# Optimization experiments

Hardware: AMD Instinct MI355X
Metric: run time of the kernel (lower is better)

## Reference

```python
import jax, jax.numpy as jnp
import numpy as np

B, T_ENC, T_DEC = 8, 1024, 100
DMODEL, H, DK, DV, DFF = 512, 8, 64, 64, 2048
L_ENC, L_DEC = 2, 2
EPS = 1e-5
MASK_FILL = -1e10  # original code masked_fills the post-softmax probs with -1e10


def _ln(x, g, b):
    m = jnp.mean(x, -1, keepdims=True)
    v = jnp.mean(jnp.square(x - m), -1, keepdims=True)
    return (x - m) * jax.lax.rsqrt(v + EPS) * g + b


def _mha(Q, K, V, Wq, Wk, Wv, causal):
    Bz, Lq, _ = Q.shape
    Lk = K.shape[1]
    q = (Q @ Wq).reshape(Bz, Lq, H, DK).transpose(0, 2, 1, 3)  # b h q d
    k = (K @ Wk).reshape(Bz, Lk, H, DK).transpose(0, 2, 1, 3)
    v = (V @ Wv).reshape(Bz, Lk, H, DV).transpose(0, 2, 1, 3)
    scores = jnp.einsum('bhqd,bhkd->bhqk', q, k) * (1.0 / np.float32(np.sqrt(DK)))
    p = jax.nn.softmax(scores, axis=-1)
    if causal:
        # faithful to original: mask applied AFTER softmax, fill value -1e10
        mask = jnp.tril(jnp.ones((Lq, Lk), dtype=bool))
        p = jnp.where(mask[None, None], p, jnp.float32(MASK_FILL))
    o = jnp.einsum('bhqk,bhkd->bhqd', p, v)
    return o.transpose(0, 2, 1, 3).reshape(Bz, Lq, H * DV)


def setup_inputs() -> dict:
    key = jax.random.key(0)
    ks = iter(jax.random.split(key, 64))
    s = 0.02
    d = {
        'x': jax.random.normal(next(ks), (B, T_ENC, DMODEL), jnp.float32),
        'y': jax.random.normal(next(ks), (B, T_DEC, DMODEL), jnp.float32),
    }
    def w(shape):
        return jax.random.normal(next(ks), shape, jnp.float32) * s
    # encoder params, stacked over layers
    d['enc_Wq'] = w((L_ENC, DMODEL, DMODEL)); d['enc_Wk'] = w((L_ENC, DMODEL, H * DK))
    d['enc_Wv'] = w((L_ENC, DMODEL, H * DV))
    d['enc_ff_w1'] = w((L_ENC, DMODEL, DFF)); d['enc_ff_b1'] = jnp.zeros((L_ENC, DFF))
    d['enc_ff_w2'] = w((L_ENC, DFF, DMODEL)); d['enc_ff_b2'] = jnp.zeros((L_ENC, DMODEL))
    d['enc_ln1_g'] = jnp.ones((L_ENC, DMODEL)); d['enc_ln1_b'] = jnp.zeros((L_ENC, DMODEL))
    d['enc_ln2_g'] = jnp.ones((L_ENC, DMODEL)); d['enc_ln2_b'] = jnp.zeros((L_ENC, DMODEL))
    # decoder params
    d['dec_Wq1'] = w((L_DEC, DMODEL, DMODEL)); d['dec_Wk1'] = w((L_DEC, DMODEL, H * DK))
    d['dec_Wv1'] = w((L_DEC, DMODEL, H * DV))
    d['dec_Wq2'] = w((L_DEC, DMODEL, DMODEL)); d['dec_Wk2'] = w((L_DEC, DMODEL, H * DK))
    d['dec_Wv2'] = w((L_DEC, DMODEL, H * DV))
    d['dec_ff_w1'] = w((L_DEC, DMODEL, DFF)); d['dec_ff_b1'] = jnp.zeros((L_DEC, DFF))
    d['dec_ff_w2'] = w((L_DEC, DFF, DMODEL)); d['dec_ff_b2'] = jnp.zeros((L_DEC, DMODEL))
    d['dec_ln1_g'] = jnp.ones((L_DEC, DMODEL)); d['dec_ln1_b'] = jnp.zeros((L_DEC, DMODEL))
    d['dec_ln2_g'] = jnp.ones((L_DEC, DMODEL)); d['dec_ln2_b'] = jnp.zeros((L_DEC, DMODEL))
    d['dec_ln3_g'] = jnp.ones((L_DEC, DMODEL)); d['dec_ln3_b'] = jnp.zeros((L_DEC, DMODEL))
    return d


def reference(x, y,
              enc_Wq, enc_Wk, enc_Wv, enc_ff_w1, enc_ff_b1, enc_ff_w2, enc_ff_b2,
              enc_ln1_g, enc_ln1_b, enc_ln2_g, enc_ln2_b,
              dec_Wq1, dec_Wk1, dec_Wv1, dec_Wq2, dec_Wk2, dec_Wv2,
              dec_ff_w1, dec_ff_b1, dec_ff_w2, dec_ff_b2,
              dec_ln1_g, dec_ln1_b, dec_ln2_g, dec_ln2_b, dec_ln3_g, dec_ln3_b):
    # encoder stacks
    for i in range(L_ENC):
        att = _mha(x, x, x, enc_Wq[i], enc_Wk[i], enc_Wv[i], causal=False)
        x1 = _ln(x + att, enc_ln1_g[i], enc_ln1_b[i])
        ff = jax.nn.relu(x1 @ enc_ff_w1[i] + enc_ff_b1[i]) @ enc_ff_w2[i] + enc_ff_b2[i]
        x = _ln(x1 + ff, enc_ln2_g[i], enc_ln2_b[i])
    # decoder stacks
    for i in range(L_DEC):
        a1 = _mha(y, y, y, dec_Wq1[i], dec_Wk1[i], dec_Wv1[i], causal=True)
        y1 = _ln(y + a1, dec_ln1_g[i], dec_ln1_b[i])
        a2 = _mha(y1, x, x, dec_Wq2[i], dec_Wk2[i], dec_Wv2[i], causal=False)
        y2 = _ln(y1 + a2, dec_ln2_g[i], dec_ln2_b[i])
        ff = jax.nn.relu(y2 @ dec_ff_w1[i] + dec_ff_b1[i]) @ dec_ff_w2[i] + dec_ff_b2[i]
        y = _ln(y2 + ff, dec_ln3_g[i], dec_ln3_b[i])
    return y
```

## Files before the change

### kernel.cpp

```cpp
#include <hip/hip_runtime.h>
#include <cstddef>

typedef unsigned short u16;
typedef __attribute__((ext_vector_type(8))) short bf16x8;
typedef __attribute__((ext_vector_type(4))) float f32x4;

__device__ __forceinline__ u16 f2b(float f) {
    union { float f; unsigned u; } x; x.f = f;
    unsigned r = x.u + 0x7FFFu + ((x.u >> 16) & 1u);
    return (u16)(r >> 16);
}
__device__ __forceinline__ float b2f(u16 v) {
    union { unsigned u; float f; } x; x.u = ((unsigned)v) << 16;
    return x.f;
}

__device__ __forceinline__ void gload_lds16(const u16* g, u16* l) {
    __builtin_amdgcn_global_load_lds(
        (const __attribute__((address_space(1))) void*)g,
        (__attribute__((address_space(3))) void*)l, 16, 0, 0);
}

__global__ __launch_bounds__(256) void gemm_mfma_kernel(
    const u16* __restrict__ A, const u16* __restrict__ Bt,
    const float* __restrict__ bias,
    float* __restrict__ Cf, u16* __restrict__ Cb,
    int M, int K, int N, int relu)
{
    __shared__ __align__(16) u16 As[128 * 32];
    __shared__ __align__(16) u16 Bs[128 * 32];

    const int tid  = threadIdx.x;
    const int wave = tid >> 6;
    const int lane = tid & 63;
    const int m0 = blockIdx.y * 128;
    const int n0 = blockIdx.x * 128;

    const int wm = (wave & 1) * 64;
    const int wn = (wave >> 1) * 64;

    const int srow  = lane >> 2;
    const int skoff = (lane & 3) * 8;

    f32x4 acc[4][4];
#pragma unroll
    for (int i = 0; i < 4; ++i)
#pragma unroll
        for (int j = 0; j < 4; ++j)
            acc[i][j] = (f32x4){0.f, 0.f, 0.f, 0.f};

    const int fm = lane & 15;
    const int fk = (lane >> 4) * 8;

    for (int k0 = 0; k0 < K; k0 += 32) {
        __syncthreads();
        {
            const int r0 = wave * 32;
            int gr0 = m0 + r0 + srow;       if (gr0 >= M) gr0 = M - 1;
            int gr1 = m0 + r0 + 16 + srow;  if (gr1 >= M) gr1 = M - 1;
            gload_lds16(A + (size_t)gr0 * K + k0 + skoff, &As[(r0) * 32]);
            gload_lds16(A + (size_t)gr1 * K + k0 + skoff, &As[(r0 + 16) * 32]);
            gload_lds16(Bt + (size_t)(n0 + r0 + srow) * K + k0 + skoff, &Bs[(r0) * 32]);
            gload_lds16(Bt + (size_t)(n0 + r0 + 16 + srow) * K + k0 + skoff, &Bs[(r0 + 16) * 32]);
        }
        __syncthreads();

        bf16x8 af[4], bfr[4];
#pragma unroll
        for (int t = 0; t < 4; ++t) {
            af[t]  = *(const bf16x8*)(&As[(wm + t * 16 + fm) * 32 + fk]);
            bfr[t] = *(const bf16x8*)(&Bs[(wn + t * 16 + fm) * 32 + fk]);
        }
#pragma unroll
        for (int i = 0; i < 4; ++i)
#pragma unroll
            for (int j = 0; j < 4; ++j)
                acc[i][j] = __builtin_amdgcn_mfma_f32_16x16x32_bf16(
                    af[i], bfr[j], acc[i][j], 0, 0, 0);
    }

    const int col = lane & 15;
    const int rq  = (lane >> 4) * 4;
#pragma unroll
    for (int j = 0; j < 4; ++j) {
        const int gn = n0 + wn + j * 16 + col;
        const float bb = bias ? bias[gn] : 0.f;
#pragma unroll
        for (int i = 0; i < 4; ++i) {
            const int gmb = m0 + wm + i * 16 + rq;
#pragma unroll
            for (int r = 0; r < 4; ++r) {
                const int gm = gmb + r;
                if (gm < M) {
                    float v = acc[i][j][r] + bb;
                    if (relu) v = fmaxf(v, 0.f);
                    if (Cb) Cb[(size_t)gm * N + gn] = f2b(v);
                    else    Cf[(size_t)gm * N + gn] = v;
                }
            }
        }
    }
}

__global__ __launch_bounds__(256) void gemm64_kernel(
    const u16* __restrict__ A, const u16* __restrict__ Bt,
    const float* __restrict__ bias,
    float* __restrict__ Cf, u16* __restrict__ Cb,
    int M, int K, int N, int relu)
{
    __shared__ __align__(16) u16 As[64 * 32];
    __shared__ __align__(16) u16 Bs[64 * 32];

    const int tid  = threadIdx.x;
    const int wave = tid >> 6;
    const int lane = tid & 63;
    const int m0 = blockIdx.y * 64;
    const int n0 = blockIdx.x * 64;
    const int wm = (wave & 1) * 32;
    const int wn = (wave >> 1) * 32;

    const int srow  = lane >> 2;
    const int skoff = (lane & 3) * 8;

    f32x4 acc[2][2];
#pragma unroll
    for (int i = 0; i < 2; ++i)
#pragma unroll
        for (int j = 0; j < 2; ++j) acc[i][j] = (f32x4){0.f, 0.f, 0.f, 0.f};

    const int fm = lane & 15;
    const int fk = (lane >> 4) * 8;

    for (int k0 = 0; k0 < K; k0 += 32) {
        __syncthreads();
        {
            int gr = m0 + wave * 16 + srow; if (gr >= M) gr = M - 1;
            gload_lds16(A + (size_t)gr * K + k0 + skoff, &As[(wave * 16) * 32]);
            gload_lds16(Bt + (size_t)(n0 + wave * 16 + srow) * K + k0 + skoff,
                        &Bs[(wave * 16) * 32]);
        }
        __syncthreads();

        bf16x8 af[2], bfr[2];
#pragma unroll
        for (int t = 0; t < 2; ++t) {
            af[t]  = *(const bf16x8*)(&As[(wm + t * 16 + fm) * 32 + fk]);
            bfr[t] = *(const bf16x8*)(&Bs[(wn + t * 16 + fm) * 32 + fk]);
        }
#pragma unroll
        for (int i = 0; i < 2; ++i)
#pragma unroll
            for (int j = 0; j < 2; ++j)
                acc[i][j] = __builtin_amdgcn_mfma_f32_16x16x32_bf16(
                    af[i], bfr[j], acc[i][j], 0, 0, 0);
    }

    const int col = lane & 15;
    const int rq  = (lane >> 4) * 4;
#pragma unroll
    for (int j = 0; j < 2; ++j) {
        const int gn = n0 + wn + j * 16 + col;
        const float bb = bias ? bias[gn] : 0.f;
#pragma unroll
        for (int i = 0; i < 2; ++i) {
            const int gmb = m0 + wm + i * 16 + rq;
#pragma unroll
            for (int r = 0; r < 4; ++r) {
                const int gm = gmb + r;
                if (gm < M) {
                    float v = acc[i][j][r] + bb;
                    if (relu) v = fmaxf(v, 0.f);
                    if (Cb) Cb[(size_t)gm * N + gn] = f2b(v);
                    else    Cf[(size_t)gm * N + gn] = v;
                }
            }
        }
    }
}

__global__ __launch_bounds__(256) void attn_mfma_kernel(
    const u16* __restrict__ Qp, const u16* __restrict__ Kp,
    const u16* __restrict__ Vp, u16* __restrict__ Op,
    int Lq, int Lk, int ldq, int ldkv, int ldo)
{
    const int q0 = blockIdx.x * 128;
    const int h  = blockIdx.y;
    const int b  = blockIdx.z;
    const int tid  = threadIdx.x;
    const int wave = tid >> 6;
    const int lane = tid & 63;
    const int c = lane & 15;
    const int g = lane >> 4;
    const float scale = 0.125f;

    __shared__ __align__(16) u16 Ks[64 * 72];
    __shared__ __align__(16) u16 Vs[64 * 72];
    __shared__ __align__(16) u16 Ps[128 * 72];

    bf16x8 aq[2][2];
#pragma unroll
    for (int half = 0; half < 2; ++half) {
        int qrow = q0 + wave * 32 + half * 16 + c;
        if (qrow > Lq - 1) qrow = Lq - 1;
        const u16* src = Qp + ((size_t)(b * Lq + qrow)) * ldq + h * 64 + g * 8;
        aq[half][0] = *(const bf16x8*)(src);
        aq[half][1] = *(const bf16x8*)(src + 32);
    }

    float den[2][4] = {};
    f32x4 o[2][4];
#pragma unroll
    for (int half = 0; half < 2; ++half)
#pragma unroll
        for (int j = 0; j < 4; ++j) o[half][j] = (f32x4){0.f, 0.f, 0.f, 0.f};

    const int srow = tid & 63;
    const int sseg = tid >> 6;

    for (int t = 0; t < (Lk >> 6); ++t) {
        const int k0 = t << 6;
        __syncthreads();
        {
            const u16* kg = Kp + ((size_t)(b * Lk + k0 + srow)) * ldkv + h * 64;
            *(bf16x8*)(&Ks[srow * 72 + sseg * 8])      = *(const bf16x8*)(kg + sseg * 8);
            *(bf16x8*)(&Ks[srow * 72 + 32 + sseg * 8]) = *(const bf16x8*)(kg + 32 + sseg * 8);
            const u16* vg = Vp + ((size_t)(b * Lk + k0 + srow)) * ldkv + h * 64;
            bf16x8 v0 = *(const bf16x8*)(vg + sseg * 8);
            bf16x8 v1 = *(const bf16x8*)(vg + 32 + sseg * 8);
#pragma unroll
            for (int i = 0; i < 8; ++i) {
                Vs[(sseg * 8 + i) * 72 + srow]      = (u16)v0[i];
                Vs[(32 + sseg * 8 + i) * 72 + srow] = (u16)v1[i];
            }
        }
        __syncthreads();

#pragma unroll
        for (int half = 0; half < 2; ++half) {
            f32x4 s[4];
#pragma unroll
            for (int jn = 0; jn < 4; ++jn) s[jn] = (f32x4){0.f, 0.f, 0.f, 0.f};
#pragma unroll
            for (int jn = 0; jn < 4; ++jn) {
                bf16x8 b0 = *(const bf16x8*)(&Ks[(jn * 16 + c) * 72 + g * 8]);
                bf16x8 b1 = *(const bf16x8*)(&Ks[(jn * 16 + c) * 72 + 32 + g * 8]);
                s[jn] = __builtin_amdgcn_mfma_f32_16x16x32_bf16(aq[half][0], b0, s[jn], 0, 0, 0);
                s[jn] = __builtin_amdgcn_mfma_f32_16x16x32_bf16(aq[half][1], b1, s[jn], 0, 0, 0);
            }
#pragma unroll
            for (int jn = 0; jn < 4; ++jn)
#pragma unroll
                for (int r = 0; r < 4; ++r) {
                    const float p = __expf(s[jn][r] * scale);
                    den[half][r] += p;
                    Ps[(wave * 32 + half * 16 + g * 4 + r) * 72 + jn * 16 + c] = f2b(p);
                }
        }

        __asm__ volatile("s_waitcnt lgkmcnt(0)" ::: "memory");

#pragma unroll
        for (int half = 0; half < 2; ++half) {
            bf16x8 ap0 = *(const bf16x8*)(&Ps[(wave * 32 + half * 16 + c) * 72 + g * 8]);
            bf16x8 ap1 = *(const bf16x8*)(&Ps[(wave * 32 + half * 16 + c) * 72 + 32 + g * 8]);
#pragma unroll
            for (int jd = 0; jd < 4; ++jd) {
                bf16x8 b0 = *(const bf16x8*)(&Vs[(jd * 16 + c) * 72 + g * 8]);
                bf16x8 b1 = *(const bf16x8*)(&Vs[(jd * 16 + c) * 72 + 32 + g * 8]);
                o[half][jd] = __builtin_amdgcn_mfma_f32_16x16x32_bf16(ap0, b0, o[half][jd], 0, 0, 0);
                o[half][jd] = __builtin_amdgcn_mfma_f32_16x16x32_bf16(ap1, b1, o[half][jd], 0, 0, 0);
            }
        }
    }

#pragma unroll
    for (int half = 0; half < 2; ++half)
#pragma unroll
        for (int r = 0; r < 4; ++r) {
#pragma unroll
            for (int msk = 1; msk < 16; msk <<= 1)
                den[half][r] += __shfl_xor(den[half][r], msk, 64);
        }

#pragma unroll
    for (int half = 0; half < 2; ++half)
#pragma unroll
        for (int r = 0; r < 4; ++r) {
            const int q = q0 + wave * 32 + half * 16 + g * 4 + r;
            if (q < Lq) {
                const float inv = 1.0f / den[half][r];
#pragma unroll
                for (int jd = 0; jd < 4; ++jd)
                    Op[((size_t)(b * Lq + q)) * ldo + h * 64 + jd * 16 + c] =
                        f2b(o[half][jd][r] * inv);
            }
        }
}

__global__ __launch_bounds__(256) void attn_split_kernel(
    const u16* __restrict__ Qp, const u16* __restrict__ Kp,
    const u16* __restrict__ Vp, float* __restrict__ Opart,
    float* __restrict__ Dpart,
    int Lq, int Lk, int ldq, int ldkv, int nsplit)
{
    const int q0 = blockIdx.x * 64;
    const int h  = blockIdx.y;
    const int b  = blockIdx.z / nsplit;
    const int sp = blockIdx.z % nsplit;
    const int tid  = threadIdx.x;
    const int wave = tid >> 6;
    const int lane = tid & 63;
    const int c = lane & 15;
    const int g = lane >> 4;
    const float scale = 0.125f;
    const int rowsTot = gridDim.z / nsplit * Lq;

    __shared__ __align__(16) u16 Ks[64 * 72];
    __shared__ __align__(16) u16 Vs[64 * 72];
    __shared__ __align__(16) u16 Ps[64 * 72];

    bf16x8 aq[2];
    {
        int qrow = q0 + wave * 16 + c;
        if (qrow > Lq - 1) qrow = Lq - 1;
        const u16* src = Qp + ((size_t)(b * Lq + qrow)) * ldq + h * 64 + g * 8;
        aq[0] = *(const bf16x8*)(src);
        aq[1] = *(const bf16x8*)(src + 32);
    }

    float den[4] = {0.f, 0.f, 0.f, 0.f};
    f32x4 o[4];
#pragma unroll
    for (int j = 0; j < 4; ++j) o[j] = (f32x4){0.f, 0.f, 0.f, 0.f};

    const int srow = tid & 63;
    const int sseg = tid >> 6;
    const int ntile = (Lk >> 6) / nsplit;

    for (int t = sp * ntile; t < (sp + 1) * ntile; ++t) {
        const int k0 = t << 6;
        __syncthreads();
        {
            const u16* kg = Kp + ((size_t)(b * Lk + k0 + srow)) * ldkv + h * 64;
            *(bf16x8*)(&Ks[srow * 72 + sseg * 8])      = *(const bf16x8*)(kg + sseg * 8);
            *(bf16x8*)(&Ks[srow * 72 + 32 + sseg * 8]) = *(const bf16x8*)(kg + 32 + sseg * 8);
            const u16* vg = Vp + ((size_t)(b * Lk + k0 + srow)) * ldkv + h * 64;
            bf16x8 v0 = *(const bf16x8*)(vg + sseg * 8);
            bf16x8 v1 = *(const bf16x8*)(vg + 32 + sseg * 8);
#pragma unroll
            for (int i = 0; i < 8; ++i) {
                Vs[(sseg * 8 + i) * 72 + srow]      = (u16)v0[i];
                Vs[(32 + sseg * 8 + i) * 72 + srow] = (u16)v1[i];
            }
        }
        __syncthreads();

        f32x4 s[4];
#pragma unroll
        for (int jn = 0; jn < 4; ++jn) s[jn] = (f32x4){0.f, 0.f, 0.f, 0.f};
#pragma unroll
        for (int jn = 0; jn < 4; ++jn) {
            bf16x8 b0 = *(const bf16x8*)(&Ks[(jn * 16 + c) * 72 + g * 8]);
            bf16x8 b1 = *(const bf16x8*)(&Ks[(jn * 16 + c) * 72 + 32 + g * 8]);
            s[jn] = __builtin_amdgcn_mfma_f32_16x16x32_bf16(aq[0], b0, s[jn], 0, 0, 0);
            s[jn] = __builtin_amdgcn_mfma_f32_16x16x32_bf16(aq[1], b1, s[jn], 0, 0, 0);
        }
#pragma unroll
        for (int jn = 0; jn < 4; ++jn)
#pragma unroll
            for (int r = 0; r < 4; ++r) {
                const float p = __expf(s[jn][r] * scale);
                den[r] += p;
                Ps[(wave * 16 + g * 4 + r) * 72 + jn * 16 + c] = f2b(p);
            }

        __asm__ volatile("s_waitcnt lgkmcnt(0)" ::: "memory");

        bf16x8 ap0 = *(const bf16x8*)(&Ps[(wave * 16 + c) * 72 + g * 8]);
        bf16x8 ap1 = *(const bf16x8*)(&Ps[(wave * 16 + c) * 72 + 32 + g * 8]);
#pragma unroll
        for (int jd = 0; jd < 4; ++jd) {
            bf16x8 b0 = *(const bf16x8*)(&Vs[(jd * 16 + c) * 72 + g * 8]);
            bf16x8 b1 = *(const bf16x8*)(&Vs[(jd * 16 + c) * 72 + 32 + g * 8]);
            o[jd] = __builtin_amdgcn_mfma_f32_16x16x32_bf16(ap0, b0, o[jd], 0, 0, 0);
            o[jd] = __builtin_amdgcn_mfma_f32_16x16x32_bf16(ap1, b1, o[jd], 0, 0, 0);
        }
    }

#pragma unroll
    for (int r = 0; r < 4; ++r) {
#pragma unroll
        for (int msk = 1; msk < 16; msk <<= 1)
            den[r] += __shfl_xor(den[r], msk, 64);
    }

#pragma unroll
    for (int r = 0; r < 4; ++r) {
        const int q = q0 + wave * 16 + g * 4 + r;
        if (q < Lq) {
            const size_t prow = (size_t)sp * rowsTot + b * Lq + q;
#pragma unroll
            for (int jd = 0; jd < 4; ++jd)
                Opart[prow * 512 + h * 64 + jd * 16 + c] = o[jd][r];
            if (c == 0) Dpart[prow * 8 + h] = den[r];
        }
    }
}

__global__ __launch_bounds__(256) void attn_combine_kernel(
    const float* __restrict__ Opart, const float* __restrict__ Dpart,
    u16* __restrict__ Out, int rows, int nsplit)
{
    const int idx = blockIdx.x * 256 + threadIdx.x;
    if (idx >= rows * 512) return;
    const int row = idx >> 9;
    const int col = idx & 511;
    const int h = col >> 6;
    float so = 0.f, sd = 0.f;
    for (int s = 0; s < nsplit; ++s) {
        so += Opart[((size_t)s * rows + row) * 512 + col];
        sd += Dpart[((size_t)s * rows + row) * 8 + h];
    }
    Out[(size_t)row * 512 + col] = f2b(so / sd);
}

__global__ __launch_bounds__(256) void wtrans_kernel(
    const float* __restrict__ W, u16* __restrict__ Wt, int K, int N, int ostride)
{
    __shared__ float t[32][33];
    const float* Wl = W + (size_t)blockIdx.z * K * N;
    u16* Wtl = Wt + (size_t)blockIdx.z * ostride;
    const int k0 = blockIdx.y * 32, n0 = blockIdx.x * 32;
    const int tr = threadIdx.x >> 3;
    const int tc = (threadIdx.x & 7) * 4;
    float4 v = *(const float4*)(Wl + (size_t)(k0 + tr) * N + n0 + tc);
    t[tr][tc] = v.x; t[tr][tc + 1] = v.y; t[tr][tc + 2] = v.z; t[tr][tc + 3] = v.w;
    __syncthreads();
    ushort4 o;
    o.x = f2b(t[tc + 0][tr]); o.y = f2b(t[tc + 1][tr]);
    o.z = f2b(t[tc + 2][tr]); o.w = f2b(t[tc + 3][tr]);
    *(ushort4*)(Wtl + (size_t)(n0 + tr) * K + k0 + tc) = o;
}

__global__ __launch_bounds__(256) void f2b_kernel(
    const float* __restrict__ X, u16* __restrict__ Y, int n)
{
    const int i = (blockIdx.x * 256 + threadIdx.x) * 8;
    if (i < n) {
        float4 a = *(const float4*)(X + i);
        float4 b = *(const float4*)(X + i + 4);
        ushort4 o0, o1;
        o0.x = f2b(a.x); o0.y = f2b(a.y); o0.z = f2b(a.z); o0.w = f2b(a.w);
        o1.x = f2b(b.x); o1.y = f2b(b.y); o1.z = f2b(b.z); o1.w = f2b(b.w);
        *(ushort4*)(Y + i) = o0;
        *(ushort4*)(Y + i + 4) = o1;
    }
}

#define MAX_LK 1024

__global__ __launch_bounds__(256) void attn_kernel(
    const float* __restrict__ Qb, const float* __restrict__ Kb,
    const float* __restrict__ Vb, float* __restrict__ Ob,
    int Lq, int Lk, int ldin, int ldo, int causal)
{
    const int q = blockIdx.x;
    const int h = blockIdx.y;
    const int b = blockIdx.z;
    const int tid = threadIdx.x;
    const float scale = 0.125f;

    __shared__ float qv[64];
    __shared__ float sc[MAX_LK];
    __shared__ float red[256];
    __shared__ float part[256];

    const float* qrow = Qb + ((size_t)(b * Lq + q)) * ldin + h * 64;
    if (tid < 64) qv[tid] = qrow[tid];
    __syncthreads();

    float lmax = -3.0e38f;
    for (int k = tid; k < Lk; k += 256) {
        const float* krow = Kb + ((size_t)(b * Lk + k)) * ldin + h * 64;
        float acc = 0.f;
#pragma unroll
        for (int d = 0; d < 64; d += 4) {
            float4 kv = *(const float4*)(krow + d);
            float4 qq = *(const float4*)(&qv[d]);
            acc = fmaf(qq.x, kv.x, acc);
            acc = fmaf(qq.y, kv.y, acc);
            acc = fmaf(qq.z, kv.z, acc);
            acc = fmaf(qq.w, kv.w, acc);
        }
        acc *= scale;
        sc[k] = acc;
        lmax = fmaxf(lmax, acc);
    }
    red[tid] = lmax;
    __syncthreads();
    for (int s = 128; s > 0; s >>= 1) {
        if (tid < s) red[tid] = fmaxf(red[tid], red[tid + s]);
        __syncthreads();
    }
    const float gmax = red[0];
    __syncthreads();

    float lsum = 0.f;
    for (int k = tid; k < Lk; k += 256) {
        float e = __expf(sc[k] - gmax);
        sc[k] = e;
        lsum += e;
    }
    red[tid] = lsum;
    __syncthreads();
    for (int s = 128; s > 0; s >>= 1) {
        if (tid < s) red[tid] += red[tid + s];
        __syncthreads();
    }
    const float inv = 1.0f / red[0];
    __syncthreads();

    const int d = tid & 63;
    const int c = tid >> 6;
    float acc = 0.f;
    for (int k = c; k < Lk; k += 4) {
        float p = sc[k] * inv;
        if (causal && k > q) p = -1.0e10f;
        acc = fmaf(p, Vb[((size_t)(b * Lk + k)) * ldin + h * 64 + d], acc);
    }
    part[tid] = acc;
    __syncthreads();
    if (tid < 64) {
        float o = part[tid] + part[tid + 64] + part[tid + 128] + part[tid + 192];
        Ob[((size_t)(b * Lq + q)) * ldo + h * 64 + tid] = o;
    }
}

__global__ __launch_bounds__(256) void ln_kernel(
    const float* __restrict__ Xf, const u16* __restrict__ Xb,
    const float* __restrict__ R,
    const float* __restrict__ g, const float* __restrict__ beta,
    float* __restrict__ O, u16* __restrict__ Ob, int nrows)
{
    const int row = blockIdx.x * 4 + (threadIdx.x >> 6);
    const int lane = threadIdx.x & 63;
    if (row >= nrows) return;
    const size_t base = (size_t)row * 512 + lane * 8;

    float v[8];
    if (Xf) {
        float4 a = *(const float4*)(Xf + base);
        float4 b = *(const float4*)(Xf + base + 4);
        v[0] = a.x; v[1] = a.y; v[2] = a.z; v[3] = a.w;
        v[4] = b.x; v[5] = b.y; v[6] = b.z; v[7] = b.w;
    } else {
        bf16x8 xb = *(const bf16x8*)(Xb + base);
#pragma unroll
        for (int i = 0; i < 8; ++i) v[i] = b2f((u16)xb[i]);
    }
    {
        float4 a = *(const float4*)(R + base);
        float4 b = *(const float4*)(R + base + 4);
        v[0] += a.x; v[1] += a.y; v[2] += a.z; v[3] += a.w;
        v[4] += b.x; v[5] += b.y; v[6] += b.z; v[7] += b.w;
    }

    float sum = 0.f;
#pragma unroll
    for (int i = 0; i < 8; ++i) sum += v[i];
#pragma unroll
    for (int msk = 1; msk < 64; msk <<= 1) sum += __shfl_xor(sum, msk, 64);
    const float mean = sum * (1.0f / 512.0f);

    float var = 0.f;
#pragma unroll
    for (int i = 0; i < 8; ++i) { v[i] -= mean; var += v[i] * v[i]; }
#pragma unroll
    for (int msk = 1; msk < 64; msk <<= 1) var += __shfl_xor(var, msk, 64);
    const float rstd = rsqrtf(var * (1.0f / 512.0f) + 1e-5f);

    float o[8];
#pragma unroll
    for (int i = 0; i < 8; ++i)
        o[i] = v[i] * rstd * g[lane * 8 + i] + beta[lane * 8 + i];

    *(float4*)(O + base)     = make_float4(o[0], o[1], o[2], o[3]);
    *(float4*)(O + base + 4) = make_float4(o[4], o[5], o[6], o[7]);
    if (Ob) {
        bf16x8 ob;
#pragma unroll
        for (int i = 0; i < 8; ++i) ob[i] = (short)f2b(o[i]);
        *(bf16x8*)(Ob + base) = ob;
    }
}

extern "C" void kernel_launch(void* const* d_in, const int* in_sizes, int n_in,
                              void* d_out, int out_size, void* d_ws, size_t ws_size,
                              hipStream_t stream)
{
    const int B = 8, T_ENC = 1024, T_DEC = 100, DM = 512, DFF = 2048;
    const int ME = B * T_ENC;
    const int MD = B * T_DEC;
    const int L = 2;
    const int NSPLIT = 4;

    int idx = 0;
    const float* x0    = (const float*)d_in[idx++];
    const float* y0    = (const float*)d_in[idx++];
    const float* eWq   = (const float*)d_in[idx++];
    const float* eWk   = (const float*)d_in[idx++];
    const float* eWv   = (const float*)d_in[idx++];
    const float* eW1   = (const float*)d_in[idx++];
    const float* eB1   = (const float*)d_in[idx++];
    const float* eW2   = (const float*)d_in[idx++];
    const float* eB2   = (const float*)d_in[idx++];
    const float* eLn1g = (const float*)d_in[idx++];
    const float* eLn1b = (const float*)d_in[idx++];
    const float* eLn2g = (const float*)d_in[idx++];
    const float* eLn2b = (const float*)d_in[idx++];
    const float* dWq1  = (const float*)d_in[idx++];
    const float* dWk1  = (const float*)d_in[idx++];
    const float* dWv1  = (const float*)d_in[idx++];
    const float* dWq2  = (const float*)d_in[idx++];
    const float* dWk2  = (const float*)d_in[idx++];
    const float* dWv2  = (const float*)d_in[idx++];
    const float* dW1   = (const float*)d_in[idx++];
    const float* dB1   = (const float*)d_in[idx++];
    const float* dW2   = (const float*)d_in[idx++];
    const float* dB2   = (const float*)d_in[idx++];
    const float* dLn1g = (const float*)d_in[idx++];
    const float* dLn1b = (const float*)d_in[idx++];
    const float* dLn2g = (const float*)d_in[idx++];
    const float* dLn2b = (const float*)d_in[idx++];
    const float* dLn3g = (const float*)d_in[idx++];
    const float* dLn3b = (const float*)d_in[idx++];

    float* ws = (float*)d_ws;
    u16* OV    = (u16*)ws;
    u16* QKVb  = OV;
    u16* H1b   = OV;
    u16* CKVb  = OV;
    u16* AFb    = (u16*)(ws + 8388608);
    float* Dpart = ws + 8388608;
    float* X1   = ws + 10485760;
    float* XOUT = ws + 14680064;
    float* DQKV  = ws + 18874368;
    float* DA    = ws + 20103168;
    float* Opart = ws + 18874368;
    float* Y1   = ws + 20512768;
    float* Y2   = ws + 20922368;
    float* YOUT = ws + 21331968;
    u16* ub  = (u16*)(ws + 21741568);
    u16* XBc = ub;
    u16* YB  = ub + 4194304;
    u16* Y1b = ub + 4603904;
    u16* Y2b = ub + 5013504;
    u16* DQb = ub + 5423104;
    u16* DAb = ub + 5832704;
    u16* DHb = ub + 6242304;
    u16* WB  = ub + 7880704;

    u16* eQKVT  = WB;
    u16* eW1T   = WB + 1572864;
    u16* eW2T   = WB + 3670016;
    u16* dQKV1T = WB + 5767168;
    u16* dWq2T  = WB + 7340032;
    u16* dKV2T  = WB + 7864320;
    u16* dW1T   = WB + 8912896;
    u16* dW2T   = WB + 11010048;

    auto wtrans = [&](const float* W, u16* Wt, int K, int N, int os) {
        hipLaunchKernelGGL(wtrans_kernel, dim3(N / 32, K / 32, L), dim3(256), 0, stream,
                           W, Wt, K, N, os);
    };
    auto conv = [&](const float* X, u16* Y, int n) {
        hipLaunchKernelGGL(f2b_kernel, dim3(n / 8 / 256), dim3(256), 0, stream, X, Y, n);
    };
    auto gemm = [&](const u16* A, const u16* Bt, const float* bias, float* Cf, u16* Cb,
                    int M, int K, int N, int relu) {
        dim3 grid(N / 128, (M + 127) / 128);
        hipLaunchKernelGGL(gemm_mfma_kernel, grid, dim3(256), 0, stream,
                           A, Bt, bias, Cf, Cb, M, K, N, relu);
    };
    auto gemm64 = [&](const u16* A, const u16* Bt, const float* bias, float* Cf, u16* Cb,
                      int M, int K, int N, int relu) {
        dim3 grid(N / 64, (M + 63) / 64);
        hipLaunchKernelGGL(gemm64_kernel, grid, dim3(256), 0, stream,
                           A, Bt, bias, Cf, Cb, M, K, N, relu);
    };
    auto ln = [&](const float* Xf, const u16* Xb, const float* R, const float* g,
                  const float* bta, float* O, u16* Ob, int rows) {
        hipLaunchKernelGGL(ln_kernel, dim3(rows / 4), dim3(256), 0, stream,
                           Xf, Xb, R, g, bta, O, Ob, rows);
    };

    wtrans(eWq,  eQKVT + 0,      DM, DM, 786432);
    wtrans(eWk,  eQKVT + 262144, DM, DM, 786432);
    wtrans(eWv,  eQKVT + 524288, DM, DM, 786432);
    wtrans(eW1,  eW1T,  DM, DFF, 1048576);
    wtrans(eW2,  eW2T,  DFF, DM, 1048576);
    wtrans(dWq1, dQKV1T + 0,      DM, DM, 786432);
    wtrans(dWk1, dQKV1T + 262144, DM, DM, 786432);
    wtrans(dWv1, dQKV1T + 524288, DM, DM, 786432);
    wtrans(dWq2, dWq2T, DM, DM, 262144);
    wtrans(dWk2, dKV2T + 0,      DM, DM, 524288);
    wtrans(dWv2, dKV2T + 262144, DM, DM, 524288);
    wtrans(dW1,  dW1T,  DM, DFF, 1048576);
    wtrans(dW2,  dW2T,  DFF, DM, 1048576);
    conv(x0, XBc, ME * DM);
    conv(y0, YB, MD * DM);

    const int BS = DM;
    const int B1S = DFF;

    const float* xin = x0;
    for (int i = 0; i < L; ++i) {
        gemm(XBc, eQKVT + (size_t)i * 786432, nullptr, nullptr, QKVb, ME, DM, 1536, 0);
        {
            dim3 grid(T_ENC / 128, 8, B);
            hipLaunchKernelGGL(attn_mfma_kernel, grid, dim3(256), 0, stream,
                               QKVb, QKVb + 512, QKVb + 1024, AFb,
                               T_ENC, T_ENC, 1536, 1536, 512);
        }
        ln(nullptr, AFb, xin, eLn1g + i * BS, eLn1b + i * BS, X1, XBc, ME);
        gemm(XBc, eW1T + (size_t)i * 1048576, eB1 + i * B1S, nullptr, H1b, ME, DM, DFF, 1);
        gemm(H1b, eW2T + (size_t)i * 1048576, eB2 + i * BS, nullptr, AFb, ME, DFF, DM, 0);
        ln(nullptr, AFb, X1, eLn2g + i * BS, eLn2b + i * BS, XOUT, XBc, ME);
        xin = XOUT;
    }

    gemm(XBc, dKV2T, nullptr, nullptr, CKVb, ME, DM, 2048, 0);

    const float* yin = y0;
    for (int i = 0; i < L; ++i) {
        gemm64(YB, dQKV1T + (size_t)i * 786432, nullptr, DQKV, nullptr, MD, DM, 1536, 0);
        {
            dim3 grid(T_DEC, 8, B);
            hipLaunchKernelGGL(attn_kernel, grid, dim3(256), 0, stream,
                               DQKV, DQKV + 512, DQKV + 1024, DA,
                               T_DEC, T_DEC, 1536, 512, 1);
        }
        ln(DA, nullptr, yin, dLn1g + i * BS, dLn1b + i * BS, Y1, Y1b, MD);
        gemm64(Y1b, dWq2T + (size_t)i * 262144, nullptr, nullptr, DQb, MD, DM, DM, 0);
        {
            dim3 grid((T_DEC + 63) / 64, 8, B * NSPLIT);
            hipLaunchKernelGGL(attn_split_kernel, grid, dim3(256), 0, stream,
                               DQb, CKVb + (size_t)i * 1024, CKVb + (size_t)i * 1024 + 512,
                               Opart, Dpart, T_DEC, T_ENC, 512, 2048, NSPLIT);
            hipLaunchKernelGGL(attn_combine_kernel, dim3(MD * 512 / 256), dim3(256), 0,
                               stream, Opart, Dpart, DAb, MD, NSPLIT);
        }
        ln(nullptr, DAb, Y1, dLn2g + i * BS, dLn2b + i * BS, Y2, Y2b, MD);
        gemm64(Y2b, dW1T + (size_t)i * 1048576, dB1 + i * B1S, nullptr, DHb, MD, DM, DFF, 1);
        gemm64(DHb, dW2T + (size_t)i * 1048576, dB2 + i * BS, DA, nullptr, MD, DFF, DM, 0);
        float* yout = (i == L - 1) ? (float*)d_out : YOUT;
        ln(DA, nullptr, Y2, dLn3g + i * BS, dLn3b + i * BS, yout,
           (i == L - 1) ? nullptr : YB, MD);
        yin = yout;
    }
}
```

Before: 928.8 us.

## Use MFMA causal attention with suffix-sum mask, fuse combine+LN, batch weight prep

```diff
diff --git a/kernel.cpp b/kernel.cpp
--- a/kernel.cpp
+++ b/kernel.cpp
@@ -295,6 +295,146 @@
                         f2b(o[half][jd][r] * inv);
             }
         }
+}
+
+__global__ __launch_bounds__(256) void attn_causal_kernel(
+    const u16* __restrict__ Qp, const u16* __restrict__ Kp,
+    const u16* __restrict__ Vp, const float* __restrict__ SuffV,
+    u16* __restrict__ Op,
+    int Lq, int Lk, int ldq, int ldkv, int ldo)
+{
+    const int q0 = blockIdx.x * 128;
+    const int h  = blockIdx.y;
+    const int b  = blockIdx.z;
+    const int tid  = threadIdx.x;
+    const int wave = tid >> 6;
+    const int lane = tid & 63;
+    const int c = lane & 15;
+    const int g = lane >> 4;
+    const float scale = 0.125f;
+
+    __shared__ __align__(16) u16 Ks[64 * 72];
+    __shared__ __align__(16) u16 Vs[64 * 72];
+    __shared__ __align__(16) u16 Ps[128 * 72];
+
+    bf16x8 aq[2][2];
+#pragma unroll
+    for (int half = 0; half < 2; ++half) {
+        int qrow = q0 + wave * 32 + half * 16 + c;
+        if (qrow > Lq - 1) qrow = Lq - 1;
+        const u16* src = Qp + ((size_t)(b * Lq + qrow)) * ldq + h * 64 + g * 8;
+        aq[half][0] = *(const bf16x8*)(src);
+        aq[half][1] = *(const bf16x8*)(src + 32);
+    }
+
+    float den[2][4] = {};
+    f32x4 o[2][4];
+#pragma unroll
+    for (int half = 0; half < 2; ++half)
+#pragma unroll
+        for (int j = 0; j < 4; ++j) o[half][j] = (f32x4){0.f, 0.f, 0.f, 0.f};
+
+    const int srow = tid & 63;
+    const int sseg = tid >> 6;
+    const int ntiles = (Lk + 63) >> 6;
+
+    for (int t = 0; t < ntiles; ++t) {
+        const int k0 = t << 6;
+        __syncthreads();
+        {
+            int kr = k0 + srow; if (kr > Lk - 1) kr = Lk - 1;
+            const u16* kg = Kp + ((size_t)(b * Lk + kr)) * ldkv + h * 64;
+            *(bf16x8*)(&Ks[srow * 72 + sseg * 8])      = *(const bf16x8*)(kg + sseg * 8);
+            *(bf16x8*)(&Ks[srow * 72 + 32 + sseg * 8]) = *(const bf16x8*)(kg + 32 + sseg * 8);
+            const u16* vg = Vp + ((size_t)(b * Lk + kr)) * ldkv + h * 64;
+            bf16x8 v0 = *(const bf16x8*)(vg + sseg * 8);
+            bf16x8 v1 = *(const bf16x8*)(vg + 32 + sseg * 8);
+#pragma unroll
+            for (int i = 0; i < 8; ++i) {
+                Vs[(sseg * 8 + i) * 72 + srow]      = (u16)v0[i];
+                Vs[(32 + sseg * 8 + i) * 72 + srow] = (u16)v1[i];
+            }
+        }
+        __syncthreads();
+
+#pragma unroll
+        for (int half = 0; half < 2; ++half) {
+            f32x4 s[4];
+#pragma unroll
+            for (int jn = 0; jn < 4; ++jn) s[jn] = (f32x4){0.f, 0.f, 0.f, 0.f};
+#pragma unroll
+            for (int jn = 0; jn < 4; ++jn) {
+                bf16x8 b0 = *(const bf16x8*)(&Ks[(jn * 16 + c) * 72 + g * 8]);
+                bf16x8 b1 = *(const bf16x8*)(&Ks[(jn * 16 + c) * 72 + 32 + g * 8]);
+                s[jn] = __builtin_amdgcn_mfma_f32_16x16x32_bf16(aq[half][0], b0, s[jn], 0, 0, 0);
+                s[jn] = __builtin_amdgcn_mfma_f32_16x16x32_bf16(aq[half][1], b1, s[jn], 0, 0, 0);
+            }
+#pragma unroll
+            for (int jn = 0; jn < 4; ++jn)
+#pragma unroll
+                for (int r = 0; r < 4; ++r) {
+                    const int kcol = k0 + jn * 16 + c;
+                    const int qrow = q0 + wave * 32 + half * 16 + g * 4 + r;
+                    const float e = __expf(s[jn][r] * scale);
+                    const float ev = (kcol < Lk) ? e : 0.f;
+                    den[half][r] += ev;
+                    const float pv = (kcol <= qrow) ? ev : 0.f;
+                    Ps[(wave * 32 + half * 16 + g * 4 + r) * 72 + jn * 16 + c] = f2b(pv);
+                }
+        }
+
+        __asm__ volatile("s_waitcnt lgkmcnt(0)" ::: "memory");
+
+#pragma unroll
+        for (int half = 0; half < 2; ++half) {
+            bf16x8 ap0 = *(const bf16x8*)(&Ps[(wave * 32 + half * 16 + c) * 72 + g * 8]);
+            bf16x8 ap1 = *(const bf16x8*)(&Ps[(wave * 32 + half * 16 + c) * 72 + 32 + g * 8]);
+#pragma unroll
+            for (int jd = 0; jd < 4; ++jd) {
+                bf16x8 b0 = *(const bf16x8*)(&Vs[(jd * 16 + c) * 72 + g * 8]);
+                bf16x8 b1 = *(const bf16x8*)(&Vs[(jd * 16 + c) * 72 + 32 + g * 8]);
+                o[half][jd] = __builtin_amdgcn_mfma_f32_16x16x32_bf16(ap0, b0, o[half][jd], 0, 0, 0);
+                o[half][jd] = __builtin_amdgcn_mfma_f32_16x16x32_bf16(ap1, b1, o[half][jd], 0, 0, 0);
+            }
+        }
+    }
+
+#pragma unroll
+    for (int half = 0; half < 2; ++half)
+#pragma unroll
+        for (int r = 0; r < 4; ++r) {
+#pragma unroll
+            for (int msk = 1; msk < 16; msk <<= 1)
+                den[half][r] += __shfl_xor(den[half][r], msk, 64);
+        }
+
+#pragma unroll
+    for (int half = 0; half < 2; ++half)
+#pragma unroll
+        for (int r = 0; r < 4; ++r) {
+            const int q = q0 + wave * 32 + half * 16 + g * 4 + r;
+            if (q < Lq) {
+                const float inv = 1.0f / den[half][r];
+                const float* sv = SuffV + ((size_t)(b * Lq + q)) * 512 + h * 64;
+#pragma unroll
+                for (int jd = 0; jd < 4; ++jd)
+                    Op[((size_t)(b * Lq + q)) * ldo + h * 64 + jd * 16 + c] =
+                        f2b(o[half][jd][r] * inv - 1.0e10f * sv[jd * 16 + c]);
+            }
+        }
+}
+
+__global__ __launch_bounds__(64) void suffv_kernel(
+    const u16* __restrict__ Vp, float* __restrict__ SuffV, int Lq, int ldv)
+{
+    const int b = blockIdx.x;
+    const int h = blockIdx.y;
+    const int d = threadIdx.x;
+    float acc = 0.f;
+    for (int q = Lq - 1; q >= 0; --q) {
+        SuffV[((size_t)(b * Lq + q)) * 512 + h * 64 + d] = acc;
+        acc += b2f(Vp[((size_t)(b * Lq + q)) * ldv + h * 64 + d]);
+    }
 }
 
 __global__ __launch_bounds__(256) void attn_split_kernel(
@@ -407,32 +547,77 @@
     }
 }
 
-__global__ __launch_bounds__(256) void attn_combine_kernel(
+__global__ __launch_bounds__(256) void combine_ln_kernel(
     const float* __restrict__ Opart, const float* __restrict__ Dpart,
-    u16* __restrict__ Out, int rows, int nsplit)
-{
-    const int idx = blockIdx.x * 256 + threadIdx.x;
-    if (idx >= rows * 512) return;
-    const int row = idx >> 9;
-    const int col = idx & 511;
-    const int h = col >> 6;
-    float so = 0.f, sd = 0.f;
+    int nsplit, int nrows,
+    const float* __restrict__ R,
+    const float* __restrict__ g, const float* __restrict__ beta,
+    float* __restrict__ O, u16* __restrict__ Ob)
+{
+    const int row = blockIdx.x * 4 + (threadIdx.x >> 6);
+    const int lane = threadIdx.x & 63;
+    if (row >= nrows) return;
+    const size_t base = (size_t)row * 512 + lane * 8;
+    const int h = lane >> 3;
+
+    float sd = 0.f;
+    float v[8] = {};
     for (int s = 0; s < nsplit; ++s) {
-        so += Opart[((size_t)s * rows + row) * 512 + col];
-        sd += Dpart[((size_t)s * rows + row) * 8 + h];
-    }
-    Out[(size_t)row * 512 + col] = f2b(so / sd);
-}
-
-__global__ __launch_bounds__(256) void wtrans_kernel(
-    const float* __restrict__ W, u16* __restrict__ Wt, int K, int N, int ostride)
+        sd += Dpart[((size_t)s * nrows + row) * 8 + h];
+        const float* op = Opart + ((size_t)s * nrows + row) * 512 + lane * 8;
+        float4 a = *(const float4*)(op);
+        float4 b = *(const float4*)(op + 4);
+        v[0] += a.x; v[1] += a.y; v[2] += a.z; v[3] += a.w;
+        v[4] += b.x; v[5] += b.y; v[6] += b.z; v[7] += b.w;
+    }
+    const float invd = 1.0f / sd;
+    {
+        float4 a = *(const float4*)(R + base);
+        float4 b = *(const float4*)(R + base + 4);
+        v[0] = v[0] * invd + a.x; v[1] = v[1] * invd + a.y;
+        v[2] = v[2] * invd + a.z; v[3] = v[3] * invd + a.w;
+        v[4] = v[4] * invd + b.x; v[5] = v[5] * invd + b.y;
+        v[6] = v[6] * invd + b.z; v[7] = v[7] * invd + b.w;
+    }
+
+    float sum = 0.f;
+#pragma unroll
+    for (int i = 0; i < 8; ++i) sum += v[i];
+#pragma unroll
+    for (int msk = 1; msk < 64; msk <<= 1) sum += __shfl_xor(sum, msk, 64);
+    const float mean = sum * (1.0f / 512.0f);
+
+    float var = 0.f;
+#pragma unroll
+    for (int i = 0; i < 8; ++i) { v[i] -= mean; var += v[i] * v[i]; }
+#pragma unroll
+    for (int msk = 1; msk < 64; msk <<= 1) var += __shfl_xor(var, msk, 64);
+    const float rstd = rsqrtf(var * (1.0f / 512.0f) + 1e-5f);
+
+    float o[8];
+#pragma unroll
+    for (int i = 0; i < 8; ++i)
+        o[i] = v[i] * rstd * g[lane * 8 + i] + beta[lane * 8 + i];
+
+    *(float4*)(O + base)     = make_float4(o[0], o[1], o[2], o[3]);
+    *(float4*)(O + base + 4) = make_float4(o[4], o[5], o[6], o[7]);
+    if (Ob) {
+        bf16x8 ob;
+#pragma unroll
+        for (int i = 0; i < 8; ++i) ob[i] = (short)f2b(o[i]);
+        *(bf16x8*)(Ob + base) = ob;
+    }
+}
+
+struct WT9 { const float* src[9]; unsigned dst[9]; unsigned os[9]; };
+struct WT4 { const float* src[4]; unsigned dst[4]; int K[4]; int N[4]; };
+
+__device__ __forceinline__ void wtrans_tile(
+    const float* Wl, u16* Wtl, int K, int N, int k0, int n0, int tid)
 {
     __shared__ float t[32][33];
-    const float* Wl = W + (size_t)blockIdx.z * K * N;
-    u16* Wtl = Wt + (size_t)blockIdx.z * ostride;
-    const int k0 = blockIdx.y * 32, n0 = blockIdx.x * 32;
-    const int tr = threadIdx.x >> 3;
-    const int tc = (threadIdx.x & 7) * 4;
+    const int tr = tid >> 3;
+    const int tc = (tid & 7) * 4;
     float4 v = *(const float4*)(Wl + (size_t)(k0 + tr) * N + n0 + tc);
     t[tr][tc] = v.x; t[tr][tc + 1] = v.y; t[tr][tc + 2] = v.z; t[tr][tc + 3] = v.w;
     __syncthreads();
@@ -442,98 +627,43 @@
     *(ushort4*)(Wtl + (size_t)(n0 + tr) * K + k0 + tc) = o;
 }
 
-__global__ __launch_bounds__(256) void f2b_kernel(
-    const float* __restrict__ X, u16* __restrict__ Y, int n)
-{
-    const int i = (blockIdx.x * 256 + threadIdx.x) * 8;
-    if (i < n) {
-        float4 a = *(const float4*)(X + i);
-        float4 b = *(const float4*)(X + i + 4);
-        ushort4 o0, o1;
-        o0.x = f2b(a.x); o0.y = f2b(a.y); o0.z = f2b(a.z); o0.w = f2b(a.w);
-        o1.x = f2b(b.x); o1.y = f2b(b.y); o1.z = f2b(b.z); o1.w = f2b(b.w);
-        *(ushort4*)(Y + i) = o0;
-        *(ushort4*)(Y + i + 4) = o1;
-    }
-}
-
-#define MAX_LK 1024
-
-__global__ __launch_bounds__(256) void attn_kernel(
-    const float* __restrict__ Qb, const float* __restrict__ Kb,
-    const float* __restrict__ Vb, float* __restrict__ Ob,
-    int Lq, int Lk, int ldin, int ldo, int causal)
-{
-    const int q = blockIdx.x;
-    const int h = blockIdx.y;
-    const int b = blockIdx.z;
-    const int tid = threadIdx.x;
-    const float scale = 0.125f;
-
-    __shared__ float qv[64];
-    __shared__ float sc[MAX_LK];
-    __shared__ float red[256];
-    __shared__ float part[256];
-
-    const float* qrow = Qb + ((size_t)(b * Lq + q)) * ldin + h * 64;
-    if (tid < 64) qv[tid] = qrow[tid];
-    __syncthreads();
-
-    float lmax = -3.0e38f;
-    for (int k = tid; k < Lk; k += 256) {
-        const float* krow = Kb + ((size_t)(b * Lk + k)) * ldin + h * 64;
-        float acc = 0.f;
-#pragma unroll
-        for (int d = 0; d < 64; d += 4) {
-            float4 kv = *(const float4*)(krow + d);
-            float4 qq = *(const float4*)(&qv[d]);
-            acc = fmaf(qq.x, kv.x, acc);
-            acc = fmaf(qq.y, kv.y, acc);
-            acc = fmaf(qq.z, kv.z, acc);
-            acc = fmaf(qq.w, kv.w, acc);
-        }
-        acc *= scale;
-        sc[k] = acc;
-        lmax = fmaxf(lmax, acc);
-    }
-    red[tid] = lmax;
-    __syncthreads();
-    for (int s = 128; s > 0; s >>= 1) {
-        if (tid < s) red[tid] = fmaxf(red[tid], red[tid + s]);
-        __syncthreads();
-    }
-    const float gmax = red[0];
-    __syncthreads();
-
-    float lsum = 0.f;
-    for (int k = tid; k < Lk; k += 256) {
-        float e = __expf(sc[k] - gmax);
-        sc[k] = e;
-        lsum += e;
-    }
-    red[tid] = lsum;
-    __syncthreads();
-    for (int s = 128; s > 0; s >>= 1) {
-        if (tid < s) red[tid] += red[tid + s];
-        __syncthreads();
-    }
-    const float inv = 1.0f / red[0];
-    __syncthreads();
-
-    const int d = tid & 63;
-    const int c = tid >> 6;
-    float acc = 0.f;
-    for (int k = c; k < Lk; k += 4) {
-        float p = sc[k] * inv;
-        if (causal && k > q) p = -1.0e10f;
-        acc = fmaf(p, Vb[((size_t)(b * Lk + k)) * ldin + h * 64 + d], acc);
-    }
-    part[tid] = acc;
-    __syncthreads();
-    if (tid < 64) {
-        float o = part[tid] + part[tid + 64] + part[tid + 128] + part[tid + 192];
-        Ob[((size_t)(b * Lq + q)) * ldo + h * 64 + tid] = o;
-    }
+__global__ __launch_bounds__(256) void wtrans9_kernel(WT9 d, u16* __restrict__ WB)
+{
+    const int w = blockIdx.z >> 1;
+    const int layer = blockIdx.z & 1;
+    const float* Wl = d.src[w] + (size_t)layer * 512 * 512;
+    u16* Wtl = WB + d.dst[w] + (size_t)layer * d.os[w];
+    wtrans_tile(Wl, Wtl, 512, 512, blockIdx.y * 32, blockIdx.x * 32, threadIdx.x);
+}
+
+__global__ __launch_bounds__(256) void wtrans4_kernel(WT4 d, u16* __restrict__ WB)
+{
+    const int w = blockIdx.z >> 1;
+    const int layer = blockIdx.z & 1;
+    const int K = d.K[w], N = d.N[w];
+    const int k0 = blockIdx.y * 32, n0 = blockIdx.x * 32;
+    if (k0 >= K || n0 >= N) return;
+    const float* Wl = d.src[w] + (size_t)layer * K * N;
+    u16* Wtl = WB + d.dst[w] + (size_t)layer * 1048576;
+    wtrans_tile(Wl, Wtl, K, N, k0, n0, threadIdx.x);
+}
+
+__global__ __launch_bounds__(256) void conv2_kernel(
+    const float* __restrict__ X0, u16* __restrict__ Y0, int n0,
+    const float* __restrict__ X1, u16* __restrict__ Y1, int n1)
+{
+    int i = (blockIdx.x * 256 + threadIdx.x) * 8;
+    const float* X; u16* Y;
+    if (i < n0) { X = X0 + i; Y = Y0 + i; }
+    else if (i < n0 + n1) { X = X1 + (i - n0); Y = Y1 + (i - n0); }
+    else return;
+    float4 a = *(const float4*)(X);
+    float4 b = *(const float4*)(X + 4);
+    ushort4 o0, o1;
+    o0.x = f2b(a.x); o0.y = f2b(a.y); o0.z = f2b(a.z); o0.w = f2b(a.w);
+    o1.x = f2b(b.x); o1.y = f2b(b.y); o1.z = f2b(b.z); o1.w = f2b(b.w);
+    *(ushort4*)(Y) = o0;
+    *(ushort4*)(Y + 4) = o1;
 }
 
 __global__ __launch_bounds__(256) void ln_kernel(
@@ -644,9 +774,9 @@
     float* Dpart = ws + 8388608;
     float* X1   = ws + 10485760;
     float* XOUT = ws + 14680064;
-    float* DQKV  = ws + 18874368;
-    float* DA    = ws + 20103168;
+    float* SuffV = ws + 18874368;
     float* Opart = ws + 18874368;
+    float* DA    = ws + 20512768 - 409600;
     float* Y1   = ws + 20512768;
     float* Y2   = ws + 20922368;
     float* YOUT = ws + 21331968;
@@ -658,24 +788,13 @@
     u16* DQb = ub + 5423104;
     u16* DAb = ub + 5832704;
     u16* DHb = ub + 6242304;
+    u16* DQKVb = DHb;
     u16* WB  = ub + 7880704;
 
-    u16* eQKVT  = WB;
-    u16* eW1T   = WB + 1572864;
-    u16* eW2T   = WB + 3670016;
-    u16* dQKV1T = WB + 5767168;
-    u16* dWq2T  = WB + 7340032;
-    u16* dKV2T  = WB + 7864320;
-    u16* dW1T   = WB + 8912896;
-    u16* dW2T   = WB + 11010048;
-
-    auto wtrans = [&](const float* W, u16* Wt, int K, int N, int os) {
-        hipLaunchKernelGGL(wtrans_kernel, dim3(N / 32, K / 32, L), dim3(256), 0, stream,
-                           W, Wt, K, N, os);
-    };
-    auto conv = [&](const float* X, u16* Y, int n) {
-        hipLaunchKernelGGL(f2b_kernel, dim3(n / 8 / 256), dim3(256), 0, stream, X, Y, n);
-    };
+    const unsigned eQKVT = 0, eW1T = 1572864, eW2T = 3670016,
+                   dQKV1T = 5767168, dWq2T = 7340032, dKV2T = 7864320,
+                   dW1T = 8912896, dW2T = 11010048;
+
     auto gemm = [&](const u16* A, const u16* Bt, const float* bias, float* Cf, u16* Cb,
                     int M, int K, int N, int relu) {
         dim3 grid(N / 128, (M + 127) / 128);
@@ -690,32 +809,40 @@
     };
     auto ln = [&](const float* Xf, const u16* Xb, const float* R, const float* g,
                   const float* bta, float* O, u16* Ob, int rows) {
-        hipLaunchKernelGGL(ln_kernel, dim3(rows / 4), dim3(256), 0, stream,
+        hipLaunchKernelGGL(ln_kernel, dim3((rows + 3) / 4), dim3(256), 0, stream,
                            Xf, Xb, R, g, bta, O, Ob, rows);
     };
 
-    wtrans(eWq,  eQKVT + 0,      DM, DM, 786432);
-    wtrans(eWk,  eQKVT + 262144, DM, DM, 786432);
-    wtrans(eWv,  eQKVT + 524288, DM, DM, 786432);
-    wtrans(eW1,  eW1T,  DM, DFF, 1048576);
-    wtrans(eW2,  eW2T,  DFF, DM, 1048576);
-    wtrans(dWq1, dQKV1T + 0,      DM, DM, 786432);
-    wtrans(dWk1, dQKV1T + 262144, DM, DM, 786432);
-    wtrans(dWv1, dQKV1T + 524288, DM, DM, 786432);
-    wtrans(dWq2, dWq2T, DM, DM, 262144);
-    wtrans(dWk2, dKV2T + 0,      DM, DM, 524288);
-    wtrans(dWv2, dKV2T + 262144, DM, DM, 524288);
-    wtrans(dW1,  dW1T,  DM, DFF, 1048576);
-    wtrans(dW2,  dW2T,  DFF, DM, 1048576);
-    conv(x0, XBc, ME * DM);
-    conv(y0, YB, MD * DM);
+    {
+        WT9 w9;
+        const float* s9[9] = {eWq, eWk, eWv, dWq1, dWk1, dWv1, dWq2, dWk2, dWv2};
+        const unsigned d9[9] = {eQKVT, eQKVT + 262144, eQKVT + 524288,
+                                dQKV1T, dQKV1T + 262144, dQKV1T + 524288,
+                                dWq2T, dKV2T, dKV2T + 262144};
+        const unsigned o9[9] = {786432, 786432, 786432, 786432, 786432, 786432,
+                                262144, 524288, 524288};
+        for (int i = 0; i < 9; ++i) { w9.src[i] = s9[i]; w9.dst[i] = d9[i]; w9.os[i] = o9[i]; }
+        hipLaunchKernelGGL(wtrans9_kernel, dim3(16, 16, 18), dim3(256), 0, stream, w9, WB);
+
+        WT4 w4;
+        const float* s4[4] = {eW1, eW2, dW1, dW2};
+        const unsigned d4[4] = {eW1T, eW2T, dW1T, dW2T};
+        const int K4[4] = {512, 2048, 512, 2048};
+        const int N4[4] = {2048, 512, 2048, 512};
+        for (int i = 0; i < 4; ++i) { w4.src[i] = s4[i]; w4.dst[i] = d4[i]; w4.K[i] = K4[i]; w4.N[i] = N4[i]; }
+        hipLaunchKernelGGL(wtrans4_kernel, dim3(64, 64, 8), dim3(256), 0, stream, w4, WB);
+
+        const int n0 = ME * DM, n1 = MD * DM;
+        hipLaunchKernelGGL(conv2_kernel, dim3((n0 + n1) / 8 / 256), dim3(256), 0, stream,
+                           x0, XBc, n0, y0, YB, n1);
+    }
 
     const int BS = DM;
     const int B1S = DFF;
 
     const float* xin = x0;
     for (int i = 0; i < L; ++i) {
-        gemm(XBc, eQKVT + (size_t)i * 786432, nullptr, nullptr, QKVb, ME, DM, 1536, 0);
+        gemm(XBc, WB + eQKVT + (size_t)i * 786432, nullptr, nullptr, QKVb, ME, DM, 1536, 0);
         {
             dim3 grid(T_ENC / 128, 8, B);
             hipLaunchKernelGGL(attn_mfma_kernel, grid, dim3(256), 0, stream,
@@ -723,36 +850,38 @@
                                T_ENC, T_ENC, 1536, 1536, 512);
         }
         ln(nullptr, AFb, xin, eLn1g + i * BS, eLn1b + i * BS, X1, XBc, ME);
-        gemm(XBc, eW1T + (size_t)i * 1048576, eB1 + i * B1S, nullptr, H1b, ME, DM, DFF, 1);
-        gemm(H1b, eW2T + (size_t)i * 1048576, eB2 + i * BS, nullptr, AFb, ME, DFF, DM, 0);
+        gemm(XBc, WB + eW1T + (size_t)i * 1048576, eB1 + i * B1S, nullptr, H1b, ME, DM, DFF, 1);
+        gemm(H1b, WB + eW2T + (size_t)i * 1048576, eB2 + i * BS, nullptr, AFb, ME, DFF, DM, 0);
         ln(nullptr, AFb, X1, eLn2g + i * BS, eLn2b + i * BS, XOUT, XBc, ME);
         xin = XOUT;
     }
 
-    gemm(XBc, dKV2T, nullptr, nullptr, CKVb, ME, DM, 2048, 0);
+    gemm(XBc, WB + dKV2T, nullptr, nullptr, CKVb, ME, DM, 2048, 0);
 
     const float* yin = y0;
     for (int i = 0; i < L; ++i) {
-        gemm64(YB, dQKV1T + (size_t)i * 786432, nullptr, DQKV, nullptr, MD, DM, 1536, 0);
+        gemm64(YB, WB + dQKV1T + (size_t)i * 786432, nullptr, nullptr, DQKVb, MD, DM, 1536, 0);
+        hipLaunchKernelGGL(suffv_kernel, dim3(B, 8), dim3(64), 0, stream,
+                           DQKVb + 1024, SuffV, T_DEC, 1536);
         {
-            dim3 grid(T_DEC, 8, B);
-            hipLaunchKernelGGL(attn_kernel, grid, dim3(256), 0, stream,
-                               DQKV, DQKV + 512, DQKV + 1024, DA,
-                               T_DEC, T_DEC, 1536, 512, 1);
-        }
-        ln(DA, nullptr, yin, dLn1g + i * BS, dLn1b + i * BS, Y1, Y1b, MD);
-        gemm64(Y1b, dWq2T + (size_t)i * 262144, nullptr, nullptr, DQb, MD, DM, DM, 0);
+            dim3 grid((T_DEC + 127) / 128, 8, B);
+            hipLaunchKernelGGL(attn_causal_kernel, grid, dim3(256), 0, stream,
+                               DQKVb, DQKVb + 512, DQKVb + 1024, SuffV, DAb,
+                               T_DEC, T_DEC, 1536, 1536, 512);
+        }
+        ln(nullptr, DAb, yin, dLn1g + i * BS, dLn1b + i * BS, Y1, Y1b, MD);
+        gemm64(Y1b, WB + dWq2T + (size_t)i * 262144, nullptr, nullptr, DQb, MD, DM, DM, 0);
         {
             dim3 grid((T_DEC + 63) / 64, 8, B * NSPLIT);
             hipLaunchKernelGGL(attn_split_kernel, grid, dim3(256), 0, stream,
                                DQb, CKVb + (size_t)i * 1024, CKVb + (size_t)i * 1024 + 512,
                                Opart, Dpart, T_DEC, T_ENC, 512, 2048, NSPLIT);
-            hipLaunchKernelGGL(attn_combine_kernel, dim3(MD * 512 / 256), dim3(256), 0,
-                               stream, Opart, Dpart, DAb, MD, NSPLIT);
-        }
-        ln(nullptr, DAb, Y1, dLn2g + i * BS, dLn2b + i * BS, Y2, Y2b, MD);
-        gemm64(Y2b, dW1T + (size_t)i * 1048576, dB1 + i * B1S, nullptr, DHb, MD, DM, DFF, 1);
-        gemm64(DHb, dW2T + (size_t)i * 1048576, dB2 + i * BS, DA, nullptr, MD, DFF, DM, 0);
+            hipLaunchKernelGGL(combine_ln_kernel, dim3((MD + 3) / 4), dim3(256), 0, stream,
+                               Opart, Dpart, NSPLIT, MD,
+                               Y1, dLn2g + i * BS, dLn2b + i * BS, Y2, Y2b);
+        }
+        gemm64(Y2b, WB + dW1T + (size_t)i * 1048576, dB1 + i * B1S, nullptr, DHb, MD, DM, DFF, 1);
+        gemm64(DHb, WB + dW2T + (size_t)i * 1048576, dB2 + i * BS, DA, nullptr, MD, DFF, DM, 0);
         float* yout = (i == L - 1) ? (float*)d_out : YOUT;
         ln(DA, nullptr, Y2, dLn3g + i * BS, dLn3b + i * BS, yout,
            (i == L - 1) ? nullptr : YB, MD);
```

Measured after the change: 858.3 us. -7.6%, faster.
